# Optimization experiments

Hardware: AMD Instinct MI355X
Metric: run time of the kernel (lower is better)

## Reference

```python
import jax, jax.numpy as jnp
import numpy as np

N_FREQ = 5
LOCALITY_RATIO = 4.0 / 7.0


def sin_emb(x, n_freq=N_FREQ):
    # x: [N, 3] -> [N, 3 + 3*2*n_freq] = [N, 33]
    freqs = 2.0 ** jnp.arange(n_freq, dtype=x.dtype)  # [1,2,4,8,16]
    parts = [x]
    for f in freqs:
        parts.append(jnp.sin(f * x))
        parts.append(jnp.cos(f * x))
    return jnp.concatenate(parts, axis=1)


def linear(x, w, b):
    # torch convention: w [out, in]
    return x @ w.T + b


def setup_inputs() -> dict:
    key = jax.random.key(0)
    ks = jax.random.split(key, 32)
    K, P, Z = 8, 131072, 64
    D_IN = 97  # 33 pos-emb + 64 slot feat
    s = 0.05
    inp = {
        "sampling_coor_fg": jax.random.normal(ks[0], (K, P, 3), jnp.float32) * 0.3,
        "z_slots": jax.random.normal(ks[1], (K, Z), jnp.float32),
        "fg_transform": jax.random.normal(ks[2], (1, 3, 3), jnp.float32),
        "fg_slot_position": jax.random.normal(ks[3], (K, 3), jnp.float32) * 0.3,
        "w_b0": jax.random.normal(ks[4], (Z, D_IN), jnp.float32) * s,
        "b_b0": jax.random.normal(ks[5], (Z,), jnp.float32) * s,
        "w_b1": jax.random.normal(ks[6], (Z, Z), jnp.float32) * s,
        "b_b1": jax.random.normal(ks[7], (Z,), jnp.float32) * s,
        "w_b2": jax.random.normal(ks[8], (Z, Z), jnp.float32) * s,
        "b_b2": jax.random.normal(ks[9], (Z,), jnp.float32) * s,
        "w_a0": jax.random.normal(ks[10], (Z, Z + D_IN), jnp.float32) * s,
        "b_a0": jax.random.normal(ks[11], (Z,), jnp.float32) * s,
        "w_a1": jax.random.normal(ks[12], (Z, Z), jnp.float32) * s,
        "b_a1": jax.random.normal(ks[13], (Z,), jnp.float32) * s,
        "w_a2": jax.random.normal(ks[14], (Z, Z), jnp.float32) * s,
        "b_a2": jax.random.normal(ks[15], (Z,), jnp.float32) * s,
        "w_lat": jax.random.normal(ks[16], (Z, Z), jnp.float32) * s,
        "b_lat": jax.random.normal(ks[17], (Z,), jnp.float32) * s,
        "w_shape": jax.random.normal(ks[18], (1, Z), jnp.float32) * s,
        "b_shape": jax.random.normal(ks[19], (1,), jnp.float32) * s,
        "w_c0": jax.random.normal(ks[20], (Z // 4, Z), jnp.float32) * s,
        "b_c0": jax.random.normal(ks[21], (Z // 4,), jnp.float32) * s,
        "w_c1": jax.random.normal(ks[22], (3, Z // 4), jnp.float32) * s,
        "b_c1": jax.random.normal(ks[23], (3,), jnp.float32) * s,
    }
    return inp


def reference(sampling_coor_fg, z_slots, fg_transform, fg_slot_position,
              w_b0, b_b0, w_b1, b_b1, w_b2, b_b2,
              w_a0, b_a0, w_a1, b_a1, w_a2, b_a2,
              w_lat, b_lat, w_shape, b_shape,
              w_c0, b_c0, w_c1, b_c1):
    K, P, _ = sampling_coor_fg.shape
    T = fg_transform[0]  # [3,3]

    # locality mask computed on transform of ORIGINAL (non-relative) coords
    coor_tmp = jnp.einsum('ij,kpj->kpi', T, sampling_coor_fg)
    outsider_idx = jnp.any(jnp.abs(coor_tmp) > LOCALITY_RATIO, axis=-1)  # [K,P]

    # rel_pos + invariant: subtract slot positions, then transform
    coor = sampling_coor_fg - fg_slot_position[:, None, :]
    coor = jnp.einsum('ij,kpj->kpi', T, coor)

    coor_flat = coor.reshape(K * P, 3)
    query = sin_emb(coor_flat)                                  # [KP, 33]
    z_ex = jnp.broadcast_to(z_slots[:, None, :], (K, P, z_slots.shape[1])).reshape(K * P, -1)
    input_fg = jnp.concatenate([query, z_ex], axis=1)           # [KP, 97]

    h = jax.nn.relu(linear(input_fg, w_b0, b_b0))
    h = jax.nn.relu(linear(h, w_b1, b_b1))
    h = jax.nn.relu(linear(h, w_b2, b_b2))
    h = jax.nn.relu(linear(jnp.concatenate([input_fg, h], axis=1), w_a0, b_a0))
    h = jax.nn.relu(linear(h, w_a1, b_a1))
    tmp = jax.nn.relu(linear(h, w_a2, b_a2))

    latent_fg = linear(tmp, w_lat, b_lat)                       # [KP, 64]
    c = jax.nn.relu(linear(latent_fg, w_c0, b_c0))
    fg_raw_rgb = linear(c, w_c1, b_c1).reshape(K, P, 3)
    fg_raw_shape = linear(tmp, w_shape, b_shape).reshape(K, P)

    # locality: zero density outside the object scale
    fg_raw_shape = jnp.where(outsider_idx, 0.0, fg_raw_shape)

    raw_masks = jax.nn.relu(fg_raw_shape)[..., None]            # [K,P,1]
    masks = raw_masks / (raw_masks.sum(axis=0) + 1e-5)          # normalize over slots
    raw_rgb = (jnp.tanh(fg_raw_rgb) + 1.0) / 2.0
    raw_sigma = raw_masks                                       # dens_noise = 0.0
    unmasked_raws = jnp.concatenate([raw_rgb, raw_sigma], axis=2)  # [K,P,4]
    masked_raws = unmasked_raws * masks
    raws = masked_raws.sum(axis=0)                              # [P,4]
    return (raws, masked_raws, unmasked_raws, masks)
```

## Files before the change

kernel.cpp:

```cpp
#include <hip/hip_runtime.h>
#include <math.h>

#define KSLOTS 8
#define PN     131072
#define LOC_RATIO 0.5714285714285714f
#define INV2048 4.8828125e-4f
#define RPS    68
#define QST    42

typedef _Float16 f16x8 __attribute__((ext_vector_type(8)));
typedef __fp16 pk16x2 __attribute__((ext_vector_type(2)));
typedef float floatx4 __attribute__((ext_vector_type(4)));
union F4H8 { int4 i; f16x8 h; };
union PK2I { pk16x2 h; int i; };

#define MFMA(A_,B_,C_) __builtin_amdgcn_mfma_f32_16x16x32_f16(A_,B_,C_,0,0,0)

#define EB_B0   0
#define EB_B1   4
#define EB_B2   12
#define EB_A0Q  20
#define EB_A0H  24
#define EB_A1   32
#define EB_A2   40
#define EB_LAT  48
#define EB_C0   58
#define WS_ZB0  30720
#define WS_ZA0  31232
#define WS_BST  31744
#define WS_W32  32096

#define OFF_RAWS     0
#define OFF_MASKED   524288
#define OFF_UNMASK   4718592
#define OFF_MASKS    8912896

#define L_AH0  0
#define L_AH1  544
#define L_CC0  1088
#define L_CC1  1408
#define L_Q32  1728
#define L_OUTS 1760
#define L_SIG  1792
#define LROW   1824

__global__ void prep_kernel(const float* __restrict__ z_slots,
                            const float* __restrict__ w_b0, const float* __restrict__ b_b0,
                            const float* __restrict__ w_b1, const float* __restrict__ b_b1,
                            const float* __restrict__ w_b2, const float* __restrict__ b_b2,
                            const float* __restrict__ w_a0, const float* __restrict__ b_a0,
                            const float* __restrict__ w_a1, const float* __restrict__ b_a1,
                            const float* __restrict__ w_a2, const float* __restrict__ b_a2,
                            const float* __restrict__ w_lat, const float* __restrict__ b_lat,
                            const float* __restrict__ w_sh, const float* __restrict__ b_sh,
                            const float* __restrict__ w_c0, const float* __restrict__ b_c0,
                            float* __restrict__ ws) {
    const int tid = blockIdx.x * blockDim.x + threadIdx.x;
    if (tid < 61440) {
        const int et = tid >> 3;
        const int j  = tid & 7;
        const int lane = et & 63;
        const int term = (et >> 6) & 1;
        const int e    = et >> 7;
        int u, nt, ks;
        if      (e < 4)  { u = 0; nt = e;            ks = 0; }
        else if (e < 12) { u = 1; nt = (e-4)  >> 1;  ks = (e-4)  & 1; }
        else if (e < 20) { u = 2; nt = (e-12) >> 1;  ks = (e-12) & 1; }
        else if (e < 24) { u = 3; nt = e - 20;       ks = 0; }
        else if (e < 32) { u = 4; nt = (e-24) >> 1;  ks = (e-24) & 1; }
        else if (e < 40) { u = 5; nt = (e-32) >> 1;  ks = (e-32) & 1; }
        else if (e < 48) { u = 6; nt = (e-40) >> 1;  ks = (e-40) & 1; }
        else if (e < 58) { u = 7; nt = (e-48) >> 1;  ks = (e-48) & 1; }
        else             { u = 8; nt = 0;            ks = e - 58; }
        const int jo = nt * 16 + (lane & 15);
        const int quad = lane >> 4;
        const int k = ks * 32 + quad * 8 + j;
        float w = 0.0f;
        switch (u) {
            case 0: w = w_b0[jo * 97 + k]; break;
            case 1: w = w_b1[jo * 64 + k]; break;
            case 2: w = w_b2[jo * 64 + k]; break;
            case 3: w = w_a0[jo * 161 + k]; break;
            case 4: w = w_a0[jo * 161 + 97 + k]; break;
            case 5: w = w_a1[jo * 64 + k]; break;
            case 6: w = w_a2[jo * 64 + k]; break;
            case 7: w = (jo < 64) ? w_lat[jo * 64 + k]
                      : ((jo == 64) ? w_sh[k] : 0.0f); break;
            default: w = w_c0[jo * 64 + k]; break;
        }
        const _Float16 hi = (_Float16)w;
        const _Float16 res = (term == 0) ? hi : (_Float16)((w - (float)hi) * 2048.0f);
        ((unsigned short*)ws)[et * 8 + j] = __builtin_bit_cast(unsigned short, res);
    } else if (tid < 65536) {
        const int idx = tid - 61440;
        const int o = idx >> 3;
        const int s = idx & 7;
        const int k = o >> 6, j = o & 63;
        float p0 = 0.0f, p1 = 0.0f;
#pragma unroll
        for (int t = 0; t < 8; ++t) {
            const int i = s * 8 + t;
            const float zv = z_slots[k * 64 + i];
            p0 = fmaf(w_b0[j * 97 + 33 + i], zv, p0);
            p1 = fmaf(w_a0[j * 161 + 33 + i], zv, p1);
        }
        p0 += __shfl_xor(p0, 1); p1 += __shfl_xor(p1, 1);
        p0 += __shfl_xor(p0, 2); p1 += __shfl_xor(p1, 2);
        p0 += __shfl_xor(p0, 4); p1 += __shfl_xor(p1, 4);
        if (s == 0) {
            ws[WS_ZB0 + o] = p0 + b_b0[j];
            ws[WS_ZA0 + o] = p1 + b_a0[j];
        }
    } else if (tid < 65888) {
        const int idx = tid - 65536;
        float v;
        if      (idx < 64)  v = b_b1[idx];
        else if (idx < 128) v = b_b2[idx - 64];
        else if (idx < 192) v = b_a1[idx - 128];
        else if (idx < 256) v = b_a2[idx - 192];
        else if (idx < 336) { const int j = idx - 256; v = (j < 64) ? b_lat[j] : ((j == 64) ? b_sh[0] : 0.0f); }
        else                v = b_c0[idx - 336];
        ws[WS_BST + idx] = v;
    } else if (tid < 66016) {
        const int idx = tid - 65888;
        const int j = idx & 63;
        ws[WS_W32 + idx] = (idx < 64) ? w_b0[j * 97 + 32] : w_a0[j * 161 + 32];
    }
}

__device__ __forceinline__ f16x8 rdfrag(const int* plane, int addr, unsigned sel) {
    const int4 a = *(const int4*)(plane + addr);
    const int4 b = *(const int4*)(plane + addr + 4);
    F4H8 u;
    u.i.x = __builtin_amdgcn_perm(a.y, a.x, sel);
    u.i.y = __builtin_amdgcn_perm(a.w, a.z, sel);
    u.i.z = __builtin_amdgcn_perm(b.y, b.x, sel);
    u.i.w = __builtin_amdgcn_perm(b.w, b.z, sel);
    return u.h;
}

__device__ __forceinline__ f16x8 as_h8(int4 v) { F4H8 u; u.i = v; return u.h; }

__device__ __forceinline__ int pkrtz_i(float a, float b) {
    PK2I u;
    u.h = __builtin_amdgcn_cvt_pkrtz(a, b);
    return u.i;
}

__device__ __forceinline__ void st_hi(int* AHw, int addr, floatx4 v) {
    AHw[addr]       = pkrtz_i(v[0], v[1]);
    AHw[addr + RPS] = pkrtz_i(v[2], v[3]);
}

__device__ __forceinline__ void st_h16(int* QHw, int rp, int halfsel, int feat, float v) {
    ((unsigned short*)QHw)[(rp * QST + feat) * 2 + halfsel] =
        __builtin_bit_cast(unsigned short, (_Float16)v);
}

__device__ __forceinline__ void unitHiDual(int* AH0, int* AH1,
                                           const int4* Bp, int ebase,
                                           const float* __restrict__ bias,
                                           f16x8 th0, f16x8 th1, f16x8 uh0, f16x8 uh1,
                                           int lane, int n, int wrA) {
    int4 B[8];
    floatx4 ac0[4], ac1[4];
#pragma unroll
    for (int nt = 0; nt < 4; ++nt) {
        B[nt*2+0] = Bp[((ebase + nt*2)*2 + 0) * 64 + lane];
        B[nt*2+1] = Bp[((ebase + nt*2)*2 + 2) * 64 + lane];
    }
    __builtin_amdgcn_s_setprio(1);
#pragma unroll
    for (int nt = 0; nt < 4; ++nt) {
        const float bv = bias[nt * 16 + n];
        const f16x8 bh0 = as_h8(B[nt*2+0]), bh1 = as_h8(B[nt*2+1]);
        ac0[nt] = (floatx4){bv, bv, bv, bv};
        ac1[nt] = (floatx4){bv, bv, bv, bv};
        ac0[nt] = MFMA(th0, bh0, ac0[nt]); ac0[nt] = MFMA(th1, bh1, ac0[nt]);
        ac1[nt] = MFMA(uh0, bh0, ac1[nt]); ac1[nt] = MFMA(uh1, bh1, ac1[nt]);
    }
    __builtin_amdgcn_s_setprio(0);
#pragma unroll
    for (int nt = 0; nt < 4; ++nt) {
        floatx4 v0, v1;
#pragma unroll
        for (int r = 0; r < 4; ++r) {
            v0[r] = fmaxf(ac0[nt][r], 0.0f);
            v1[r] = fmaxf(ac1[nt][r], 0.0f);
        }
        st_hi(AH0, wrA + nt * 16, v0);
        st_hi(AH1, wrA + nt * 16, v1);
    }
}

__global__ __launch_bounds__(128, 3)
void fg_kernel(const float* __restrict__ coor_in,
               const float* __restrict__ fg_transform,
               const float* __restrict__ fg_slot_pos,
               const float* __restrict__ w_c1, const float* __restrict__ b_c1,
               const float* __restrict__ ws,
               float* __restrict__ out) {
    __shared__ int LB[2][LROW];
    const int lane = threadIdx.x & 63;
    const int wv   = threadIdx.x >> 6;
    const int tile = blockIdx.x * 2 + wv;
    const int kk = tile >> 12;
    const int p0 = (tile & 4095) << 5;

    int* AH0 = LB[wv] + L_AH0;
    int* AH1 = LB[wv] + L_AH1;
    float* Q32w  = (float*)(LB[wv] + L_Q32);
    float* OUTSw = (float*)(LB[wv] + L_OUTS);
    float* SIGw  = (float*)(LB[wv] + L_SIG);
    float* CC0   = (float*)(LB[wv] + L_CC0);
    float* CC1   = (float*)(LB[wv] + L_CC1);

    const int* ws_i = (const int*)ws;
    const int4* Bp = (const int4*)ws_i;
    const int n = lane & 15, quad = lane >> 4;
    const unsigned sel = (n & 1) ? 0x07060302u : 0x05040100u;
    const int rdA = (n >> 1) * RPS + quad * 8;
    const int rdQ = (n >> 1) * QST + quad * 8;
    const int wrA = (2 * quad) * RPS + n;

#pragma unroll
    for (int t = 0; t < 2; ++t) {
        int* QHt = LB[wv] + t * 544;
        const int p = n;
        const int role = quad;
        const long idx3 = ((long)kk * PN + p0 + t * 16 + p) * 3;
        const float x = coor_in[idx3 + 0];
        const float y = coor_in[idx3 + 1];
        const float zc = coor_in[idx3 + 2];
        const float T00 = fg_transform[0], T01 = fg_transform[1], T02 = fg_transform[2];
        const float T10 = fg_transform[3], T11 = fg_transform[4], T12 = fg_transform[5];
        const float T20 = fg_transform[6], T21 = fg_transform[7], T22 = fg_transform[8];
        if (role < 3) {
            const float px = fg_slot_pos[kk*3+0], py = fg_slot_pos[kk*3+1], pz = fg_slot_pos[kk*3+2];
            const float rx = x - px, ry = y - py, rz = zc - pz;
            const float cx = T00*rx + T01*ry + T02*rz;
            const float cy = T10*rx + T11*ry + T12*rz;
            const float cz = T20*rx + T21*ry + T22*rz;
            const float c = (role == 0) ? cx : ((role == 1) ? cy : cz);
            const int rp = p >> 1;
            const int hs = p & 1;
            st_h16(QHt, rp, hs, role, c);
            const float rev = c * 0.15915494309189535f;
            const float fr = rev - floorf(rev);
            float s  = __builtin_amdgcn_sinf(fr);
            float co = __builtin_amdgcn_cosf(fr);
#pragma unroll
            for (int l = 0; l < 5; ++l) {
                st_h16(QHt, rp, hs, 3 + 6*l + role, s);
                if (l == 4 && role == 2) {
                    Q32w[t * 16 + p] = co;
                } else {
                    st_h16(QHt, rp, hs, 6 + 6*l + role, co);
                }
                if (l < 4) {
                    const float tt = s * co;
                    const float s2 = s * s;
                    co = fmaf(-2.0f, s2, 1.0f);
                    s  = tt + tt;
                }
            }
        } else {
            const float o0 = T00*x + T01*y + T02*zc;
            const float o1 = T10*x + T11*y + T12*zc;
            const float o2 = T20*x + T21*y + T22*zc;
            const bool outs = (fabsf(o0) > LOC_RATIO) || (fabsf(o1) > LOC_RATIO) || (fabsf(o2) > LOC_RATIO);
            OUTSw[t * 16 + p] = outs ? 1.0f : 0.0f;
        }
    }

    const f16x8 qh_0 = rdfrag(LB[wv] + 0,   rdQ, sel);
    const f16x8 qh_1 = rdfrag(LB[wv] + 544, rdQ, sel);

    {
        const float* zb0 = ws + WS_ZB0 + kk * 64;
        const float* w32p = ws + WS_W32;
        int4 B[4];
#pragma unroll
        for (int nt = 0; nt < 4; ++nt) {
            B[nt] = Bp[((EB_B0 + nt)*2 + 0) * 64 + lane];
        }
#pragma unroll
        for (int nt = 0; nt < 4; ++nt) {
            const float bv = zb0[nt * 16 + n];
            const float w32 = w32p[nt * 16 + n];
            const f16x8 bh = as_h8(B[nt]);
            floatx4 ac0 = {bv, bv, bv, bv};
            floatx4 ac1 = {bv, bv, bv, bv};
            __builtin_amdgcn_s_setprio(1);
            ac0 = MFMA(qh_0, bh, ac0);
            ac1 = MFMA(qh_1, bh, ac1);
            __builtin_amdgcn_s_setprio(0);
            floatx4 v0, v1;
#pragma unroll
            for (int r = 0; r < 4; ++r) {
                v0[r] = fmaxf(fmaf(w32, Q32w[quad*4+r],    ac0[r]), 0.0f);
                v1[r] = fmaxf(fmaf(w32, Q32w[16+quad*4+r], ac1[r]), 0.0f);
            }
            st_hi(AH0, wrA + nt * 16, v0);
            st_hi(AH1, wrA + nt * 16, v1);
        }
    }

    f16x8 th0, th1, uh0, uh1;
#define RD_H() do { \
        th0 = rdfrag(AH0, rdA, sel);      th1 = rdfrag(AH0, rdA + 32, sel); \
        uh0 = rdfrag(AH1, rdA, sel);      uh1 = rdfrag(AH1, rdA + 32, sel); \
    } while (0)

    RD_H(); unitHiDual(AH0, AH1, Bp, EB_B1, ws + WS_BST + 0,   th0, th1, uh0, uh1, lane, n, wrA);
    RD_H(); unitHiDual(AH0, AH1, Bp, EB_B2, ws + WS_BST + 64,  th0, th1, uh0, uh1, lane, n, wrA);

    RD_H();
    {
        const float* za0 = ws + WS_ZA0 + kk * 64;
        const float* w32p = ws + WS_W32 + 64;
        floatx4 ac0[4], ac1[4];
        int4 B[8];
#pragma unroll
        for (int nt = 0; nt < 4; ++nt) {
            B[nt] = Bp[((EB_A0Q + nt)*2 + 0) * 64 + lane];
        }
        __builtin_amdgcn_s_setprio(1);
#pragma unroll
        for (int nt = 0; nt < 4; ++nt) {
            const float bv = za0[nt * 16 + n];
            const f16x8 bh = as_h8(B[nt]);
            ac0[nt] = (floatx4){bv, bv, bv, bv};
            ac1[nt] = (floatx4){bv, bv, bv, bv};
            ac0[nt] = MFMA(qh_0, bh, ac0[nt]);
            ac1[nt] = MFMA(qh_1, bh, ac1[nt]);
        }
        __builtin_amdgcn_s_setprio(0);
#pragma unroll
        for (int nt = 0; nt < 4; ++nt) {
            B[nt*2+0] = Bp[((EB_A0H + nt*2)*2 + 0) * 64 + lane];
            B[nt*2+1] = Bp[((EB_A0H + nt*2)*2 + 2) * 64 + lane];
        }
        __builtin_amdgcn_s_setprio(1);
#pragma unroll
        for (int nt = 0; nt < 4; ++nt) {
            const f16x8 bh0 = as_h8(B[nt*2+0]), bh1 = as_h8(B[nt*2+1]);
            ac0[nt] = MFMA(th0, bh0, ac0[nt]); ac0[nt] = MFMA(th1, bh1, ac0[nt]);
            ac1[nt] = MFMA(uh0, bh0, ac1[nt]); ac1[nt] = MFMA(uh1, bh1, ac1[nt]);
        }
        __builtin_amdgcn_s_setprio(0);
#pragma unroll
        for (int nt = 0; nt < 4; ++nt) {
            const float w32 = w32p[nt * 16 + n];
            floatx4 v0, v1;
#pragma unroll
            for (int r = 0; r < 4; ++r) {
                v0[r] = fmaxf(fmaf(w32, Q32w[quad*4+r],    ac0[nt][r]), 0.0f);
                v1[r] = fmaxf(fmaf(w32, Q32w[16+quad*4+r], ac1[nt][r]), 0.0f);
            }
            st_hi(AH0, wrA + nt * 16, v0);
            st_hi(AH1, wrA + nt * 16, v1);
        }
    }

    RD_H(); unitHiDual(AH0, AH1, Bp, EB_A1, ws + WS_BST + 128, th0, th1, uh0, uh1, lane, n, wrA);
    RD_H(); unitHiDual(AH0, AH1, Bp, EB_A2, ws + WS_BST + 192, th0, th1, uh0, uh1, lane, n, wrA);

    RD_H();
    {
        const float* bias = ws + WS_BST + 256;
        int4 B[8];
#pragma unroll
        for (int nt = 0; nt < 4; ++nt) {
            B[nt*2+0] = Bp[((EB_LAT + nt*2)*2 + 0) * 64 + lane];
            B[nt*2+1] = Bp[((EB_LAT + nt*2)*2 + 2) * 64 + lane];
        }
        __builtin_amdgcn_s_setprio(1);
#pragma unroll
        for (int nt = 0; nt < 4; ++nt) {
            const float bv = bias[nt * 16 + n];
            const f16x8 bh0 = as_h8(B[nt*2+0]), bh1 = as_h8(B[nt*2+1]);
            floatx4 a0 = {bv, bv, bv, bv}, a1 = {bv, bv, bv, bv};
            a0 = MFMA(th0, bh0, a0); a0 = MFMA(th1, bh1, a0);
            a1 = MFMA(uh0, bh0, a1); a1 = MFMA(uh1, bh1, a1);
            st_hi(AH0, wrA + nt * 16, a0);
            st_hi(AH1, wrA + nt * 16, a1);
        }
        __builtin_amdgcn_s_setprio(0);
        {
            const float bv = bias[64 + n];
            const int e0 = EB_LAT + 8;
            const f16x8 bh0 = as_h8(Bp[(e0*2+0) * 64 + lane]);
            const f16x8 bh1 = as_h8(Bp[(e0*2+2) * 64 + lane]);
            floatx4 a0 = {bv, bv, bv, bv};
            floatx4 a1 = {bv, bv, bv, bv};
            __builtin_amdgcn_s_setprio(1);
            a0 = MFMA(th0, bh0, a0); a0 = MFMA(th1, bh1, a0);
            a1 = MFMA(uh0, bh0, a1); a1 = MFMA(uh1, bh1, a1);
            __builtin_amdgcn_s_setprio(0);
            if (n == 0) {
#pragma unroll
                for (int r = 0; r < 4; ++r) {
                    SIGw[quad * 4 + r]      = a0[r];
                    SIGw[16 + quad * 4 + r] = a1[r];
                }
            }
        }
    }

    RD_H();
    {
        const float* bias = ws + WS_BST + 336;
        const float bv = bias[n];
        const f16x8 bh0 = as_h8(Bp[((EB_C0+0)*2+0) * 64 + lane]);
        const f16x8 bh1 = as_h8(Bp[((EB_C0+1)*2+0) * 64 + lane]);
        floatx4 a0 = {bv, bv, bv, bv}, a1 = {bv, bv, bv, bv};
        a0 = MFMA(th0, bh0, a0); a0 = MFMA(th1, bh1, a0);
        a1 = MFMA(uh0, bh0, a1); a1 = MFMA(uh1, bh1, a1);
#pragma unroll
        for (int r = 0; r < 4; ++r) {
            CC0[(quad * 4 + r) * 20 + n] = fmaxf(a0[r], 0.0f);
            CC1[(quad * 4 + r) * 20 + n] = fmaxf(a1[r], 0.0f);
        }
    }

#pragma unroll
    for (int t = 0; t < 2; ++t) {
        const float* CCt = t ? CC1 : CC0;
        const int p = lane >> 2, o = lane & 3;
        float v;
        if (o < 3) {
            const float* cr = CCt + p * 20;
            float a = b_c1[o];
#pragma unroll
            for (int i = 0; i < 16; ++i) a = fmaf(w_c1[o * 16 + i], cr[i], a);
            const float e = __expf(-2.0f * a);
            v = __builtin_amdgcn_rcpf(1.0f + e);
        } else {
            const float sig = SIGw[t * 16 + p];
            const float outs = OUTSw[t * 16 + p];
            v = (outs > 0.5f) ? 0.0f : fmaxf(sig, 0.0f);
        }
        const long idx = (long)kk * PN + p0 + t * 16 + p;
        out[OFF_UNMASK + (idx << 2) + o] = v;
    }
#undef RD_H
}

__global__ __launch_bounds__(256)
void compose_kernel(float* __restrict__ out) {
    const int p = blockIdx.x * blockDim.x + threadIdx.x;
    const float4* un = (const float4*)(out + OFF_UNMASK);
    float4 u[KSLOTS];
    float s = 0.0f;
#pragma unroll
    for (int k = 0; k < KSLOTS; ++k) {
        u[k] = un[k * PN + p];
        s += u[k].w;
    }
    const float inv = 1.0f / (s + 1e-5f);
    float4* mk = (float4*)(out + OFF_MASKED);
    float* ms = out + OFF_MASKS;
    float4 r = make_float4(0.f, 0.f, 0.f, 0.f);
#pragma unroll
    for (int k = 0; k < KSLOTS; ++k) {
        const float m = u[k].w * inv;
        ms[k * PN + p] = m;
        const float4 v = make_float4(u[k].x * m, u[k].y * m, u[k].z * m, u[k].w * m);
        mk[k * PN + p] = v;
        r.x += v.x; r.y += v.y; r.z += v.z; r.w += v.w;
    }
    ((float4*)(out + OFF_RAWS))[p] = r;
}

extern "C" void kernel_launch(void* const* d_in, const int* in_sizes, int n_in,
                              void* d_out, int out_size, void* d_ws, size_t ws_size,
                              hipStream_t stream) {
    const float* coor = (const float*)d_in[0];
    const float* z    = (const float*)d_in[1];
    const float* ft   = (const float*)d_in[2];
    const float* pos  = (const float*)d_in[3];
    const float* w_b0 = (const float*)d_in[4];  const float* b_b0 = (const float*)d_in[5];
    const float* w_b1 = (const float*)d_in[6];  const float* b_b1 = (const float*)d_in[7];
    const float* w_b2 = (const float*)d_in[8];  const float* b_b2 = (const float*)d_in[9];
    const float* w_a0 = (const float*)d_in[10]; const float* b_a0 = (const float*)d_in[11];
    const float* w_a1 = (const float*)d_in[12]; const float* b_a1 = (const float*)d_in[13];
    const float* w_a2 = (const float*)d_in[14]; const float* b_a2 = (const float*)d_in[15];
    const float* w_lat = (const float*)d_in[16]; const float* b_lat = (const float*)d_in[17];
    const float* w_sh  = (const float*)d_in[18]; const float* b_sh  = (const float*)d_in[19];
    const float* w_c0  = (const float*)d_in[20]; const float* b_c0  = (const float*)d_in[21];
    const float* w_c1  = (const float*)d_in[22]; const float* b_c1  = (const float*)d_in[23];
    float* out = (float*)d_out;
    float* ws  = (float*)d_ws;

    hipLaunchKernelGGL(prep_kernel, dim3(258), dim3(256), 0, stream,
                       z,
                       w_b0, b_b0, w_b1, b_b1, w_b2, b_b2,
                       w_a0, b_a0, w_a1, b_a1, w_a2, b_a2,
                       w_lat, b_lat, w_sh, b_sh, w_c0, b_c0, ws);
    hipLaunchKernelGGL(fg_kernel, dim3((KSLOTS * PN / 32) / 2), dim3(128), 0, stream,
                       coor, ft, pos, w_c1, b_c1, ws, out);
    hipLaunchKernelGGL(compose_kernel, dim3(PN / 256), dim3(256), 0, stream, out);
}
```

Measured before the change: 225.3 us.

## Process 64 points per wavefront to reuse weight fragments across four tiles

Each wavefront now handles four 16-point tiles instead of two, with one wave per block in place of two. Every weight fragment loaded from global memory then feeds four MFMA chains rather than two, halving weight-load traffic per point and giving each wave more independent MFMAs to interleave. The cost is more registers (accumulators and fragments for four tiles) and double the LDS per wave, and the launch-bounds occupancy hint of 3 is dropped, so occupancy may fall.

Result: slower. 236.9 us (+5.2%).

```diff
diff --git a/kernel.cpp b/kernel.cpp
--- a/kernel.cpp
+++ b/kernel.cpp
@@ -35,14 +35,11 @@
 #define OFF_UNMASK   4718592
 #define OFF_MASKS    8912896
 
-#define L_AH0  0
-#define L_AH1  544
-#define L_CC0  1088
-#define L_CC1  1408
-#define L_Q32  1728
-#define L_OUTS 1760
-#define L_SIG  1792
-#define LROW   1824
+#define L_CC   2176
+#define L_Q32  3456
+#define L_OUTS 3520
+#define L_SIG  3584
+#define LROW   3648
 
 __global__ void prep_kernel(const float* __restrict__ z_slots,
                             const float* __restrict__ w_b0, const float* __restrict__ b_b0,
@@ -157,66 +154,27 @@
         __builtin_bit_cast(unsigned short, (_Float16)v);
 }
 
-__device__ __forceinline__ void unitHiDual(int* AH0, int* AH1,
-                                           const int4* Bp, int ebase,
-                                           const float* __restrict__ bias,
-                                           f16x8 th0, f16x8 th1, f16x8 uh0, f16x8 uh1,
-                                           int lane, int n, int wrA) {
-    int4 B[8];
-    floatx4 ac0[4], ac1[4];
-#pragma unroll
-    for (int nt = 0; nt < 4; ++nt) {
-        B[nt*2+0] = Bp[((ebase + nt*2)*2 + 0) * 64 + lane];
-        B[nt*2+1] = Bp[((ebase + nt*2)*2 + 2) * 64 + lane];
-    }
-    __builtin_amdgcn_s_setprio(1);
-#pragma unroll
-    for (int nt = 0; nt < 4; ++nt) {
-        const float bv = bias[nt * 16 + n];
-        const f16x8 bh0 = as_h8(B[nt*2+0]), bh1 = as_h8(B[nt*2+1]);
-        ac0[nt] = (floatx4){bv, bv, bv, bv};
-        ac1[nt] = (floatx4){bv, bv, bv, bv};
-        ac0[nt] = MFMA(th0, bh0, ac0[nt]); ac0[nt] = MFMA(th1, bh1, ac0[nt]);
-        ac1[nt] = MFMA(uh0, bh0, ac1[nt]); ac1[nt] = MFMA(uh1, bh1, ac1[nt]);
-    }
-    __builtin_amdgcn_s_setprio(0);
-#pragma unroll
-    for (int nt = 0; nt < 4; ++nt) {
-        floatx4 v0, v1;
-#pragma unroll
-        for (int r = 0; r < 4; ++r) {
-            v0[r] = fmaxf(ac0[nt][r], 0.0f);
-            v1[r] = fmaxf(ac1[nt][r], 0.0f);
-        }
-        st_hi(AH0, wrA + nt * 16, v0);
-        st_hi(AH1, wrA + nt * 16, v1);
-    }
-}
-
-__global__ __launch_bounds__(128, 3)
+__global__ __launch_bounds__(64)
 void fg_kernel(const float* __restrict__ coor_in,
                const float* __restrict__ fg_transform,
                const float* __restrict__ fg_slot_pos,
                const float* __restrict__ w_c1, const float* __restrict__ b_c1,
                const float* __restrict__ ws,
                float* __restrict__ out) {
-    __shared__ int LB[2][LROW];
-    const int lane = threadIdx.x & 63;
-    const int wv   = threadIdx.x >> 6;
-    const int tile = blockIdx.x * 2 + wv;
-    const int kk = tile >> 12;
-    const int p0 = (tile & 4095) << 5;
-
-    int* AH0 = LB[wv] + L_AH0;
-    int* AH1 = LB[wv] + L_AH1;
-    float* Q32w  = (float*)(LB[wv] + L_Q32);
-    float* OUTSw = (float*)(LB[wv] + L_OUTS);
-    float* SIGw  = (float*)(LB[wv] + L_SIG);
-    float* CC0   = (float*)(LB[wv] + L_CC0);
-    float* CC1   = (float*)(LB[wv] + L_CC1);
-
-    const int* ws_i = (const int*)ws;
-    const int4* Bp = (const int4*)ws_i;
+    __shared__ int LB[LROW];
+    const int lane = threadIdx.x;
+    const int kk = blockIdx.x >> 11;
+    const int p0 = (blockIdx.x & 2047) << 6;
+
+    int* AH[4];
+#pragma unroll
+    for (int t = 0; t < 4; ++t) AH[t] = LB + t * 544;
+    float* Q32w  = (float*)(LB + L_Q32);
+    float* OUTSw = (float*)(LB + L_OUTS);
+    float* SIGw  = (float*)(LB + L_SIG);
+    float* CC    = (float*)(LB + L_CC);
+
+    const int4* Bp = (const int4*)ws;
     const int n = lane & 15, quad = lane >> 4;
     const unsigned sel = (n & 1) ? 0x07060302u : 0x05040100u;
     const int rdA = (n >> 1) * RPS + quad * 8;
@@ -224,8 +182,8 @@
     const int wrA = (2 * quad) * RPS + n;
 
 #pragma unroll
-    for (int t = 0; t < 2; ++t) {
-        int* QHt = LB[wv] + t * 544;
+    for (int t = 0; t < 4; ++t) {
+        int* QHt = LB + t * 544;
         const int p = n;
         const int role = quad;
         const long idx3 = ((long)kk * PN + p0 + t * 16 + p) * 3;
@@ -273,98 +231,120 @@
         }
     }
 
-    const f16x8 qh_0 = rdfrag(LB[wv] + 0,   rdQ, sel);
-    const f16x8 qh_1 = rdfrag(LB[wv] + 544, rdQ, sel);
+    f16x8 qh[4];
+#pragma unroll
+    for (int t = 0; t < 4; ++t) qh[t] = rdfrag(LB + t * 544, rdQ, sel);
 
     {
         const float* zb0 = ws + WS_ZB0 + kk * 64;
         const float* w32p = ws + WS_W32;
         int4 B[4];
 #pragma unroll
-        for (int nt = 0; nt < 4; ++nt) {
-            B[nt] = Bp[((EB_B0 + nt)*2 + 0) * 64 + lane];
-        }
+        for (int nt = 0; nt < 4; ++nt) B[nt] = Bp[((EB_B0 + nt)*2 + 0) * 64 + lane];
 #pragma unroll
         for (int nt = 0; nt < 4; ++nt) {
             const float bv = zb0[nt * 16 + n];
             const float w32 = w32p[nt * 16 + n];
             const f16x8 bh = as_h8(B[nt]);
-            floatx4 ac0 = {bv, bv, bv, bv};
-            floatx4 ac1 = {bv, bv, bv, bv};
+            floatx4 ac[4];
+#pragma unroll
+            for (int t = 0; t < 4; ++t) ac[t] = (floatx4){bv, bv, bv, bv};
             __builtin_amdgcn_s_setprio(1);
-            ac0 = MFMA(qh_0, bh, ac0);
-            ac1 = MFMA(qh_1, bh, ac1);
+#pragma unroll
+            for (int t = 0; t < 4; ++t) ac[t] = MFMA(qh[t], bh, ac[t]);
             __builtin_amdgcn_s_setprio(0);
-            floatx4 v0, v1;
-#pragma unroll
-            for (int r = 0; r < 4; ++r) {
-                v0[r] = fmaxf(fmaf(w32, Q32w[quad*4+r],    ac0[r]), 0.0f);
-                v1[r] = fmaxf(fmaf(w32, Q32w[16+quad*4+r], ac1[r]), 0.0f);
+#pragma unroll
+            for (int t = 0; t < 4; ++t) {
+                floatx4 v;
+#pragma unroll
+                for (int r = 0; r < 4; ++r)
+                    v[r] = fmaxf(fmaf(w32, Q32w[t*16 + quad*4 + r], ac[t][r]), 0.0f);
+                st_hi(AH[t], wrA + nt * 16, v);
             }
-            st_hi(AH0, wrA + nt * 16, v0);
-            st_hi(AH1, wrA + nt * 16, v1);
-        }
-    }
-
-    f16x8 th0, th1, uh0, uh1;
+        }
+    }
+
+    f16x8 h0[4], h1[4];
 #define RD_H() do { \
-        th0 = rdfrag(AH0, rdA, sel);      th1 = rdfrag(AH0, rdA + 32, sel); \
-        uh0 = rdfrag(AH1, rdA, sel);      uh1 = rdfrag(AH1, rdA + 32, sel); \
+        _Pragma("unroll") \
+        for (int t = 0; t < 4; ++t) { \
+            h0[t] = rdfrag(AH[t], rdA, sel); \
+            h1[t] = rdfrag(AH[t], rdA + 32, sel); \
+        } \
     } while (0)
 
-    RD_H(); unitHiDual(AH0, AH1, Bp, EB_B1, ws + WS_BST + 0,   th0, th1, uh0, uh1, lane, n, wrA);
-    RD_H(); unitHiDual(AH0, AH1, Bp, EB_B2, ws + WS_BST + 64,  th0, th1, uh0, uh1, lane, n, wrA);
+#define UNIT_HI(EBASE, BIASOFF) do { \
+        const float* bias_ = ws + WS_BST + (BIASOFF); \
+        int4 B_[8]; \
+        _Pragma("unroll") \
+        for (int nt = 0; nt < 4; ++nt) { \
+            B_[nt*2+0] = Bp[(((EBASE) + nt*2)*2 + 0) * 64 + lane]; \
+            B_[nt*2+1] = Bp[(((EBASE) + nt*2)*2 + 2) * 64 + lane]; \
+        } \
+        _Pragma("unroll") \
+        for (int nt = 0; nt < 4; ++nt) { \
+            const float bv_ = bias_[nt * 16 + n]; \
+            const f16x8 bh0_ = as_h8(B_[nt*2+0]), bh1_ = as_h8(B_[nt*2+1]); \
+            floatx4 ac_[4]; \
+            _Pragma("unroll") \
+            for (int t = 0; t < 4; ++t) ac_[t] = (floatx4){bv_, bv_, bv_, bv_}; \
+            __builtin_amdgcn_s_setprio(1); \
+            _Pragma("unroll") \
+            for (int t = 0; t < 4; ++t) { ac_[t] = MFMA(h0[t], bh0_, ac_[t]); ac_[t] = MFMA(h1[t], bh1_, ac_[t]); } \
+            __builtin_amdgcn_s_setprio(0); \
+            _Pragma("unroll") \
+            for (int t = 0; t < 4; ++t) { \
+                floatx4 v_; \
+                _Pragma("unroll") \
+                for (int r = 0; r < 4; ++r) v_[r] = fmaxf(ac_[t][r], 0.0f); \
+                st_hi(AH[t], wrA + nt * 16, v_); \
+            } \
+        } \
+    } while (0)
+
+    RD_H(); UNIT_HI(EB_B1, 0);
+    RD_H(); UNIT_HI(EB_B2, 64);
 
     RD_H();
     {
         const float* za0 = ws + WS_ZA0 + kk * 64;
         const float* w32p = ws + WS_W32 + 64;
-        floatx4 ac0[4], ac1[4];
-        int4 B[8];
+        int4 Bq[4], Bh[8];
+#pragma unroll
+        for (int nt = 0; nt < 4; ++nt) Bq[nt] = Bp[((EB_A0Q + nt)*2 + 0) * 64 + lane];
 #pragma unroll
         for (int nt = 0; nt < 4; ++nt) {
-            B[nt] = Bp[((EB_A0Q + nt)*2 + 0) * 64 + lane];
-        }
-        __builtin_amdgcn_s_setprio(1);
+            Bh[nt*2+0] = Bp[((EB_A0H + nt*2)*2 + 0) * 64 + lane];
+            Bh[nt*2+1] = Bp[((EB_A0H + nt*2)*2 + 2) * 64 + lane];
+        }
 #pragma unroll
         for (int nt = 0; nt < 4; ++nt) {
             const float bv = za0[nt * 16 + n];
-            const f16x8 bh = as_h8(B[nt]);
-            ac0[nt] = (floatx4){bv, bv, bv, bv};
-            ac1[nt] = (floatx4){bv, bv, bv, bv};
-            ac0[nt] = MFMA(qh_0, bh, ac0[nt]);
-            ac1[nt] = MFMA(qh_1, bh, ac1[nt]);
-        }
-        __builtin_amdgcn_s_setprio(0);
-#pragma unroll
-        for (int nt = 0; nt < 4; ++nt) {
-            B[nt*2+0] = Bp[((EB_A0H + nt*2)*2 + 0) * 64 + lane];
-            B[nt*2+1] = Bp[((EB_A0H + nt*2)*2 + 2) * 64 + lane];
-        }
-        __builtin_amdgcn_s_setprio(1);
-#pragma unroll
-        for (int nt = 0; nt < 4; ++nt) {
-            const f16x8 bh0 = as_h8(B[nt*2+0]), bh1 = as_h8(B[nt*2+1]);
-            ac0[nt] = MFMA(th0, bh0, ac0[nt]); ac0[nt] = MFMA(th1, bh1, ac0[nt]);
-            ac1[nt] = MFMA(uh0, bh0, ac1[nt]); ac1[nt] = MFMA(uh1, bh1, ac1[nt]);
-        }
-        __builtin_amdgcn_s_setprio(0);
-#pragma unroll
-        for (int nt = 0; nt < 4; ++nt) {
             const float w32 = w32p[nt * 16 + n];
-            floatx4 v0, v1;
-#pragma unroll
-            for (int r = 0; r < 4; ++r) {
-                v0[r] = fmaxf(fmaf(w32, Q32w[quad*4+r],    ac0[nt][r]), 0.0f);
-                v1[r] = fmaxf(fmaf(w32, Q32w[16+quad*4+r], ac1[nt][r]), 0.0f);
+            const f16x8 bq = as_h8(Bq[nt]);
+            const f16x8 bh0 = as_h8(Bh[nt*2+0]), bh1 = as_h8(Bh[nt*2+1]);
+            floatx4 ac[4];
+#pragma unroll
+            for (int t = 0; t < 4; ++t) ac[t] = (floatx4){bv, bv, bv, bv};
+            __builtin_amdgcn_s_setprio(1);
+#pragma unroll
+            for (int t = 0; t < 4; ++t) ac[t] = MFMA(qh[t], bq, ac[t]);
+#pragma unroll
+            for (int t = 0; t < 4; ++t) { ac[t] = MFMA(h0[t], bh0, ac[t]); ac[t] = MFMA(h1[t], bh1, ac[t]); }
+            __builtin_amdgcn_s_setprio(0);
+#pragma unroll
+            for (int t = 0; t < 4; ++t) {
+                floatx4 v;
+#pragma unroll
+                for (int r = 0; r < 4; ++r)
+                    v[r] = fmaxf(fmaf(w32, Q32w[t*16 + quad*4 + r], ac[t][r]), 0.0f);
+                st_hi(AH[t], wrA + nt * 16, v);
             }
-            st_hi(AH0, wrA + nt * 16, v0);
-            st_hi(AH1, wrA + nt * 16, v1);
-        }
-    }
-
-    RD_H(); unitHiDual(AH0, AH1, Bp, EB_A1, ws + WS_BST + 128, th0, th1, uh0, uh1, lane, n, wrA);
-    RD_H(); unitHiDual(AH0, AH1, Bp, EB_A2, ws + WS_BST + 192, th0, th1, uh0, uh1, lane, n, wrA);
+        }
+    }
+
+    RD_H(); UNIT_HI(EB_A1, 128);
+    RD_H(); UNIT_HI(EB_A2, 192);
 
     RD_H();
     {
@@ -375,35 +355,38 @@
             B[nt*2+0] = Bp[((EB_LAT + nt*2)*2 + 0) * 64 + lane];
             B[nt*2+1] = Bp[((EB_LAT + nt*2)*2 + 2) * 64 + lane];
         }
-        __builtin_amdgcn_s_setprio(1);
 #pragma unroll
         for (int nt = 0; nt < 4; ++nt) {
             const float bv = bias[nt * 16 + n];
             const f16x8 bh0 = as_h8(B[nt*2+0]), bh1 = as_h8(B[nt*2+1]);
-            floatx4 a0 = {bv, bv, bv, bv}, a1 = {bv, bv, bv, bv};
-            a0 = MFMA(th0, bh0, a0); a0 = MFMA(th1, bh1, a0);
-            a1 = MFMA(uh0, bh0, a1); a1 = MFMA(uh1, bh1, a1);
-            st_hi(AH0, wrA + nt * 16, a0);
-            st_hi(AH1, wrA + nt * 16, a1);
-        }
-        __builtin_amdgcn_s_setprio(0);
+            floatx4 ac[4];
+#pragma unroll
+            for (int t = 0; t < 4; ++t) ac[t] = (floatx4){bv, bv, bv, bv};
+            __builtin_amdgcn_s_setprio(1);
+#pragma unroll
+            for (int t = 0; t < 4; ++t) { ac[t] = MFMA(h0[t], bh0, ac[t]); ac[t] = MFMA(h1[t], bh1, ac[t]); }
+            __builtin_amdgcn_s_setprio(0);
+#pragma unroll
+            for (int t = 0; t < 4; ++t) st_hi(AH[t], wrA + nt * 16, ac[t]);
+        }
         {
             const float bv = bias[64 + n];
             const int e0 = EB_LAT + 8;
             const f16x8 bh0 = as_h8(Bp[(e0*2+0) * 64 + lane]);
             const f16x8 bh1 = as_h8(Bp[(e0*2+2) * 64 + lane]);
-            floatx4 a0 = {bv, bv, bv, bv};
-            floatx4 a1 = {bv, bv, bv, bv};
+            floatx4 ac[4];
+#pragma unroll
+            for (int t = 0; t < 4; ++t) ac[t] = (floatx4){bv, bv, bv, bv};
             __builtin_amdgcn_s_setprio(1);
-            a0 = MFMA(th0, bh0, a0); a0 = MFMA(th1, bh1, a0);
-            a1 = MFMA(uh0, bh0, a1); a1 = MFMA(uh1, bh1, a1);
+#pragma unroll
+            for (int t = 0; t < 4; ++t) { ac[t] = MFMA(h0[t], bh0, ac[t]); ac[t] = MFMA(h1[t], bh1, ac[t]); }
             __builtin_amdgcn_s_setprio(0);
             if (n == 0) {
 #pragma unroll
-                for (int r = 0; r < 4; ++r) {
-                    SIGw[quad * 4 + r]      = a0[r];
-                    SIGw[16 + quad * 4 + r] = a1[r];
-                }
+                for (int t = 0; t < 4; ++t)
+#pragma unroll
+                    for (int r = 0; r < 4; ++r)
+                        SIGw[t * 16 + quad * 4 + r] = ac[t][r];
             }
         }
     }
@@ -414,19 +397,23 @@
         const float bv = bias[n];
         const f16x8 bh0 = as_h8(Bp[((EB_C0+0)*2+0) * 64 + lane]);
         const f16x8 bh1 = as_h8(Bp[((EB_C0+1)*2+0) * 64 + lane]);
-        floatx4 a0 = {bv, bv, bv, bv}, a1 = {bv, bv, bv, bv};
-        a0 = MFMA(th0, bh0, a0); a0 = MFMA(th1, bh1, a0);
-        a1 = MFMA(uh0, bh0, a1); a1 = MFMA(uh1, bh1, a1);
-#pragma unroll
-        for (int r = 0; r < 4; ++r) {
-            CC0[(quad * 4 + r) * 20 + n] = fmaxf(a0[r], 0.0f);
-            CC1[(quad * 4 + r) * 20 + n] = fmaxf(a1[r], 0.0f);
-        }
-    }
-
-#pragma unroll
-    for (int t = 0; t < 2; ++t) {
-        const float* CCt = t ? CC1 : CC0;
+        floatx4 ac[4];
+#pragma unroll
+        for (int t = 0; t < 4; ++t) ac[t] = (floatx4){bv, bv, bv, bv};
+        __builtin_amdgcn_s_setprio(1);
+#pragma unroll
+        for (int t = 0; t < 4; ++t) { ac[t] = MFMA(h0[t], bh0, ac[t]); ac[t] = MFMA(h1[t], bh1, ac[t]); }
+        __builtin_amdgcn_s_setprio(0);
+#pragma unroll
+        for (int t = 0; t < 4; ++t)
+#pragma unroll
+            for (int r = 0; r < 4; ++r)
+                CC[t * 320 + (quad * 4 + r) * 20 + n] = fmaxf(ac[t][r], 0.0f);
+    }
+
+#pragma unroll
+    for (int t = 0; t < 4; ++t) {
+        const float* CCt = CC + t * 320;
         const int p = lane >> 2, o = lane & 3;
         float v;
         if (o < 3) {
@@ -445,6 +432,7 @@
         out[OFF_UNMASK + (idx << 2) + o] = v;
     }
 #undef RD_H
+#undef UNIT_HI
 }
 
 __global__ __launch_bounds__(256)
@@ -498,7 +486,7 @@
                        w_b0, b_b0, w_b1, b_b1, w_b2, b_b2,
                        w_a0, b_a0, w_a1, b_a1, w_a2, b_a2,
                        w_lat, b_lat, w_sh, b_sh, w_c0, b_c0, ws);
-    hipLaunchKernelGGL(fg_kernel, dim3((KSLOTS * PN / 32) / 2), dim3(128), 0, stream,
+    hipLaunchKernelGGL(fg_kernel, dim3(KSLOTS * PN / 64), dim3(64), 0, stream,
                        coor, ft, pos, w_c1, b_c1, ws, out);
     hipLaunchKernelGGL(compose_kernel, dim3(PN / 256), dim3(256), 0, stream, out);
 }
```
